# Optimization experiments

Hardware: AMD Instinct MI355X
Metric: run time of the kernel (lower is better)

The kernel has to match this reference:

```python
import jax, jax.numpy as jnp
import numpy as np

TEMPERATURE = 1.0
CLAMP = 10.0

def setup_inputs() -> dict:
    key = jax.random.key(0)
    k1, k2, kw, kb, km = jax.random.split(key, 5)
    B, N1, N2, D = 8, 2048, 2048, 256
    features1 = jax.random.normal(k1, (B, N1, D), dtype=jnp.float32)
    features2 = jax.random.normal(k2, (B, N2, D), dtype=jnp.float32)
    # Linear(D, D) params (torch convention: y = x @ W.T + b)
    W = jax.random.normal(kw, (D, D), dtype=jnp.float32) * (1.0 / np.sqrt(D))
    b = jax.random.normal(kb, (D,), dtype=jnp.float32) * 0.02
    # learnable metric matrix (initialized near identity, small perturbation)
    metric = jnp.eye(D, dtype=jnp.float32) + 0.01 * jax.random.normal(km, (D, D), dtype=jnp.float32)
    return {"features1": features1, "features2": features2, "W": W, "b": b, "metric": metric}

def reference(features1, features2, W, b, metric):
    # Linear transform (torch nn.Linear: x @ W.T + b)
    f1 = features1 @ W.T + b  # (B, N1, D)
    f2 = features2 @ W.T + b  # (B, N2, D)
    M = (metric + metric.T) * 0.5  # symmetrized metric (D, D)
    # Mahalanobis distance^2 expanded: d(x,y) = xMx + yMy - 2 xMy (valid since M symmetric)
    f1M = f1 @ M                                      # (B, N1, D)
    f2M = f2 @ M                                      # (B, N2, D)
    q1 = jnp.sum(f1M * f1, axis=-1)                   # (B, N1)
    q2 = jnp.sum(f2M * f2, axis=-1)                   # (B, N2)
    cross = jnp.einsum('bnd,bmd->bnm', f1M, f2)       # (B, N1, N2)
    dist_sq = q1[:, :, None] + q2[:, None, :] - 2.0 * cross
    stable = jnp.clip(-dist_sq / TEMPERATURE, -CLAMP, CLAMP)
    return jnp.exp(stable)
```

## Files before the change

kernel.cpp:

```cpp
#include <hip/hip_runtime.h>

#define DD 256
#define NROW 2048
#define TROWS 16384

typedef __attribute__((ext_vector_type(8))) short short8;
typedef __attribute__((ext_vector_type(4))) float f32x4;

__device__ __forceinline__ unsigned short f2bf(float f) {
  unsigned int u = __float_as_uint(f);
  u += 0x7FFFu + ((u >> 16) & 1u);
  return (unsigned short)(u >> 16);
}

__device__ __forceinline__ void gload_lds16(const unsigned short* g, unsigned short* l) {
  __builtin_amdgcn_global_load_lds(
      (const __attribute__((address_space(1))) unsigned int*)(const void*)g,
      (__attribute__((address_space(3))) unsigned int*)(void*)l,
      16, 0, 0);
}

__global__ void k_prep(const float* __restrict__ metric, const float* __restrict__ W,
                       const float* __restrict__ bvec,
                       unsigned short* __restrict__ Wbf, unsigned short* __restrict__ WpT,
                       float* __restrict__ bp)
{
  __shared__ float msrow[DD];
  __shared__ float red[DD];
  const int e = blockIdx.x, d = threadIdx.x;
  msrow[d] = 0.5f * (metric[e*DD + d] + metric[d*DD + e]);
  Wbf[e*DD + d] = f2bf(W[e*DD + d]);
  __syncthreads();
  float acc = 0.f;
  for (int j = 0; j < DD; ++j) acc += msrow[j] * W[j*DD + d];
  WpT[e*DD + d] = f2bf(acc);
  red[d] = msrow[d] * bvec[d];
  __syncthreads();
  for (int s = 128; s; s >>= 1) { if (d < s) red[d] += red[d + s]; __syncthreads(); }
  if (d == 0) bp[e] = red[0];
}

__global__ __launch_bounds__(256, 2)
void k_fgemm(const float* __restrict__ x1, const float* __restrict__ x2,
             const unsigned short* __restrict__ B1, const unsigned short* __restrict__ B2,
             const float* __restrict__ bb, const float* __restrict__ bpv,
             unsigned short* __restrict__ o1, unsigned short* __restrict__ o2,
             float* __restrict__ qp1, float* __restrict__ qp2)
{
  __shared__ __align__(16) unsigned short As[2][64*32];
  __shared__ __align__(16) unsigned short B1s[2][256*32];
  __shared__ __align__(16) unsigned short B2s[2][256*32];

  const int tid  = threadIdx.x;
  const int lane = tid & 63;
  const int wave = tid >> 6;
  const int row0 = blockIdx.x * 64;
  const int z    = blockIdx.y;

  const float* X       = z ? x2 : x1;
  unsigned short* outp = z ? o2 : o1;
  float* qp            = z ? qp2 : qp1;

  f32x4 accF[4][4], accM[4][4];
#pragma unroll
  for (int m = 0; m < 4; ++m)
#pragma unroll
    for (int n = 0; n < 4; ++n) { accF[m][n] = (f32x4){0,0,0,0}; accM[m][n] = (f32x4){0,0,0,0}; }

  const int ar = tid >> 2;
  const int ako = (tid & 3) * 8;
  const int lrow = lane >> 2;
  const int lkk  = (lane & 3) * 8;

#define STAGE_B(buf, k0) do { \
  _Pragma("unroll") \
  for (int c = 0; c < 4; ++c) { \
    const int chunk = wave * 4 + c; \
    const int rb = (chunk*16 + lrow)*DD + (k0) + lkk; \
    gload_lds16(B1 + rb, &B1s[buf][chunk*512]); \
    gload_lds16(B2 + rb, &B2s[buf][chunk*512]); \
  } } while (0)

#define LOAD_A(k0) \
  float4 a0 = *(const float4*)(X + (long long)(row0 + ar)*DD + (k0) + ako); \
  float4 a1 = *(const float4*)(X + (long long)(row0 + ar)*DD + (k0) + ako + 4)

#define CVT_WRITE_A(buf) do { \
  union { unsigned short us[8]; int4 v; } u; \
  u.us[0]=f2bf(a0.x); u.us[1]=f2bf(a0.y); u.us[2]=f2bf(a0.z); u.us[3]=f2bf(a0.w); \
  u.us[4]=f2bf(a1.x); u.us[5]=f2bf(a1.y); u.us[6]=f2bf(a1.z); u.us[7]=f2bf(a1.w); \
  *(int4*)&As[buf][ar*32 + ako] = u.v; } while (0)

  {
    LOAD_A(0);
    STAGE_B(0, 0);
    CVT_WRITE_A(0);
  }
  __syncthreads();

  const int lr = lane & 15;
  const int lk = (lane >> 4) * 8;

#pragma unroll
  for (int kt = 0; kt < 8; ++kt) {
    const int cur = kt & 1;
    if (kt < 7) {
      const int k0 = (kt + 1) * 32;
      LOAD_A(k0);
      STAGE_B(cur ^ 1, k0);
      short8 af[4];
#pragma unroll
      for (int m = 0; m < 4; ++m) af[m] = *(const short8*)&As[cur][(m*16 + lr)*32 + lk];
#pragma unroll
      for (int n = 0; n < 4; ++n) {
        const short8 b1 = *(const short8*)&B1s[cur][(wave*64 + n*16 + lr)*32 + lk];
        const short8 b2 = *(const short8*)&B2s[cur][(wave*64 + n*16 + lr)*32 + lk];
#pragma unroll
        for (int m = 0; m < 4; ++m) {
          accF[m][n] = __builtin_amdgcn_mfma_f32_16x16x32_bf16(af[m], b1, accF[m][n], 0, 0, 0);
          accM[m][n] = __builtin_amdgcn_mfma_f32_16x16x32_bf16(af[m], b2, accM[m][n], 0, 0, 0);
        }
      }
      CVT_WRITE_A(cur ^ 1);
    } else {
      short8 af[4];
#pragma unroll
      for (int m = 0; m < 4; ++m) af[m] = *(const short8*)&As[cur][(m*16 + lr)*32 + lk];
#pragma unroll
      for (int n = 0; n < 4; ++n) {
        const short8 b1 = *(const short8*)&B1s[cur][(wave*64 + n*16 + lr)*32 + lk];
        const short8 b2 = *(const short8*)&B2s[cur][(wave*64 + n*16 + lr)*32 + lk];
#pragma unroll
        for (int m = 0; m < 4; ++m) {
          accF[m][n] = __builtin_amdgcn_mfma_f32_16x16x32_bf16(af[m], b1, accF[m][n], 0, 0, 0);
          accM[m][n] = __builtin_amdgcn_mfma_f32_16x16x32_bf16(af[m], b2, accM[m][n], 0, 0, 0);
        }
      }
    }
    __syncthreads();
  }

  float bbv[4], bpv4[4];
#pragma unroll
  for (int n = 0; n < 4; ++n) {
    const int coll = wave*64 + n*16 + (lane & 15);
    bbv[n]  = bb[coll];
    bpv4[n] = bpv[coll];
  }
#pragma unroll
  for (int m = 0; m < 4; ++m) {
#pragma unroll
    for (int r = 0; r < 4; ++r) {
      const int rowl = m*16 + (lane >> 4)*4 + r;
      float p = 0.f;
#pragma unroll
      for (int n = 0; n < 4; ++n) {
        const int coll = wave*64 + n*16 + (lane & 15);
        const float fv  = accF[m][n][r] + bbv[n];
        const float fMv = accM[m][n][r] + bpv4[n];
        p += fv * fMv;
        outp[(long long)(row0 + rowl)*DD + coll] = f2bf(z ? fv : fMv);
      }
      p += __shfl_xor(p, 1); p += __shfl_xor(p, 2);
      p += __shfl_xor(p, 4); p += __shfl_xor(p, 8);
      if ((lane & 15) == 0) qp[wave*TROWS + row0 + rowl] = p;
    }
  }
#undef STAGE_B
#undef LOAD_A
#undef CVT_WRITE_A
}

__global__ __launch_bounds__(256, 2)
void k_cross(const unsigned short* __restrict__ f1M, const unsigned short* __restrict__ f2,
             const float* __restrict__ qp1, const float* __restrict__ qp2,
             float* __restrict__ out)
{
  __shared__ __align__(16) unsigned short As[2][128*32];
  __shared__ __align__(16) unsigned short Bs[2][128*32];
  __shared__ float q1s[128];
  __shared__ float q2s[128];

  const int tid  = threadIdx.x;
  const int lane = tid & 63;
  const int wave = tid >> 6;
  const int wr = wave >> 1;
  const int wc = wave & 1;

  const int bid = blockIdx.x;
  const int z  = bid & 7;
  const int t  = bid >> 3;
  const int bx = t & 15;
  const int by = t >> 4;
  const int row0 = by * 128;
  const int col0 = bx * 128;

  const unsigned short* A = f1M + (long long)z * NROW * DD;
  const unsigned short* B = f2  + (long long)z * NROW * DD;

  if (tid < 128) {
    const int rg = z*NROW + row0 + tid;
    q1s[tid] = qp1[rg] + qp1[TROWS + rg] + qp1[2*TROWS + rg] + qp1[3*TROWS + rg];
  } else {
    const int cg = z*NROW + col0 + (tid - 128);
    q2s[tid-128] = qp2[cg] + qp2[TROWS + cg] + qp2[2*TROWS + cg] + qp2[3*TROWS + cg];
  }

  f32x4 acc[4][4];
#pragma unroll
  for (int m = 0; m < 4; ++m)
#pragma unroll
    for (int n = 0; n < 4; ++n) acc[m][n] = (f32x4){0,0,0,0};

  const int lrow = lane >> 2;
  const int lkk  = (lane & 3) * 8;

#define STAGE_C(buf, k0) do { \
  _Pragma("unroll") \
  for (int c = 0; c < 2; ++c) { \
    const int chunk = wave * 2 + c; \
    gload_lds16(A + (long long)(row0 + chunk*16 + lrow)*DD + (k0) + lkk, &As[buf][chunk*512]); \
    gload_lds16(B + (long long)(col0 + chunk*16 + lrow)*DD + (k0) + lkk, &Bs[buf][chunk*512]); \
  } } while (0)

  STAGE_C(0, 0);
  __syncthreads();

  const int lr = lane & 15;
  const int lk = (lane >> 4) * 8;

#pragma unroll
  for (int kt = 0; kt < 8; ++kt) {
    const int cur = kt & 1;
    if (kt < 7) STAGE_C(cur ^ 1, (kt + 1) * 32);
    short8 af[4];
#pragma unroll
    for (int m = 0; m < 4; ++m) af[m] = *(const short8*)&As[cur][(wr*64 + m*16 + lr)*32 + lk];
#pragma unroll
    for (int n = 0; n < 4; ++n) {
      const short8 bfr = *(const short8*)&Bs[cur][(wc*64 + n*16 + lr)*32 + lk];
#pragma unroll
      for (int m = 0; m < 4; ++m)
        acc[m][n] = __builtin_amdgcn_mfma_f32_16x16x32_bf16(af[m], bfr, acc[m][n], 0, 0, 0);
    }
    __syncthreads();
  }

  float* outz = out + (long long)z * NROW * NROW;
#pragma unroll
  for (int m = 0; m < 4; ++m) {
#pragma unroll
    for (int r = 0; r < 4; ++r) {
      const int rowl = wr*64 + m*16 + (lane >> 4)*4 + r;
#pragma unroll
      for (int n = 0; n < 4; ++n) {
        const int coll = wc*64 + n*16 + (lane & 15);
        const float dsq = q1s[rowl] + q2s[coll] - 2.0f * acc[m][n][r];
        const float sc = fminf(fmaxf(-dsq, -10.0f), 10.0f);
        outz[(long long)(row0 + rowl)*NROW + (col0 + coll)] = __expf(sc);
      }
    }
  }
#undef STAGE_C
}

extern "C" void kernel_launch(void* const* d_in, const int* in_sizes, int n_in,
                              void* d_out, int out_size, void* d_ws, size_t ws_size,
                              hipStream_t stream) {
  const float* x1     = (const float*)d_in[0];
  const float* x2     = (const float*)d_in[1];
  const float* W      = (const float*)d_in[2];
  const float* bv     = (const float*)d_in[3];
  const float* metric = (const float*)d_in[4];
  float* out = (float*)d_out;

  if (ws_size < 20000000) return;
  unsigned short* p   = (unsigned short*)d_ws;
  unsigned short* f1M = p; p += (size_t)TROWS*DD;
  unsigned short* f2  = p; p += (size_t)TROWS*DD;
  unsigned short* Wbf = p; p += DD*DD;
  unsigned short* WpT = p; p += DD*DD;
  float* fp  = (float*)p;
  float* qp1 = fp; fp += 4*TROWS;
  float* qp2 = fp; fp += 4*TROWS;
  float* bp  = fp; fp += 256;

  k_prep<<<256, 256, 0, stream>>>(metric, W, bv, Wbf, WpT, bp);
  dim3 gf(256, 2);
  k_fgemm<<<gf, 256, 0, stream>>>(x1, x2, Wbf, WpT, bv, bp, f1M, f2, qp1, qp2);
  k_cross<<<2048, 256, 0, stream>>>(f1M, f2, qp1, qp2, out);
}
```

Before: 71.07 us.

## Merge three kernels into one persistent cooperative kernel with grid syncs

```diff
diff --git a/kernel.cpp b/kernel.cpp
--- a/kernel.cpp
+++ b/kernel.cpp
@@ -1,4 +1,7 @@
 #include <hip/hip_runtime.h>
+#include <hip/hip_cooperative_groups.h>
+
+namespace cg = cooperative_groups;
 
 #define DD 256
 #define NROW 2048
@@ -20,65 +23,56 @@
       16, 0, 0);
 }
 
-__global__ void k_prep(const float* __restrict__ metric, const float* __restrict__ W,
-                       const float* __restrict__ bvec,
-                       unsigned short* __restrict__ Wbf, unsigned short* __restrict__ WpT,
-                       float* __restrict__ bp)
+union SMem {
+  struct { float msrow[DD]; float red[DD]; } pr;
+  struct { unsigned short As[2][64*32]; unsigned short B1s[2][256*32]; unsigned short B2s[2][256*32]; } fg;
+  struct { unsigned short As[2][128*32]; unsigned short Bs[2][128*32]; float q1s[128]; float q2s[128]; } cr;
+};
+
+__global__ __launch_bounds__(256, 2)
+void k_mega(const float* x1, const float* x2, const float* W,
+            const float* bvec, const float* metric,
+            unsigned short* Wbf, unsigned short* WpT, float* bp,
+            unsigned short* f1M, unsigned short* f2,
+            float* qp1, float* qp2, float* out)
 {
-  __shared__ float msrow[DD];
-  __shared__ float red[DD];
-  const int e = blockIdx.x, d = threadIdx.x;
-  msrow[d] = 0.5f * (metric[e*DD + d] + metric[d*DD + e]);
-  Wbf[e*DD + d] = f2bf(W[e*DD + d]);
-  __syncthreads();
-  float acc = 0.f;
-  for (int j = 0; j < DD; ++j) acc += msrow[j] * W[j*DD + d];
-  WpT[e*DD + d] = f2bf(acc);
-  red[d] = msrow[d] * bvec[d];
-  __syncthreads();
-  for (int s = 128; s; s >>= 1) { if (d < s) red[d] += red[d + s]; __syncthreads(); }
-  if (d == 0) bp[e] = red[0];
-}
-
-__global__ __launch_bounds__(256, 2)
-void k_fgemm(const float* __restrict__ x1, const float* __restrict__ x2,
-             const unsigned short* __restrict__ B1, const unsigned short* __restrict__ B2,
-             const float* __restrict__ bb, const float* __restrict__ bpv,
-             unsigned short* __restrict__ o1, unsigned short* __restrict__ o2,
-             float* __restrict__ qp1, float* __restrict__ qp2)
-{
-  __shared__ __align__(16) unsigned short As[2][64*32];
-  __shared__ __align__(16) unsigned short B1s[2][256*32];
-  __shared__ __align__(16) unsigned short B2s[2][256*32];
-
+  __shared__ SMem sm;
   const int tid  = threadIdx.x;
   const int lane = tid & 63;
   const int wave = tid >> 6;
-  const int row0 = blockIdx.x * 64;
-  const int z    = blockIdx.y;
-
-  const float* X       = z ? x2 : x1;
-  unsigned short* outp = z ? o2 : o1;
-  float* qp            = z ? qp2 : qp1;
-
-  f32x4 accF[4][4], accM[4][4];
-#pragma unroll
-  for (int m = 0; m < 4; ++m)
-#pragma unroll
-    for (int n = 0; n < 4; ++n) { accF[m][n] = (f32x4){0,0,0,0}; accM[m][n] = (f32x4){0,0,0,0}; }
-
-  const int ar = tid >> 2;
-  const int ako = (tid & 3) * 8;
-  const int lrow = lane >> 2;
-  const int lkk  = (lane & 3) * 8;
+  const int nb   = gridDim.x;
+
+  for (int e = blockIdx.x; e < DD; e += nb) {
+    const int d = tid;
+    sm.pr.msrow[d] = 0.5f * (metric[e*DD + d] + metric[d*DD + e]);
+    Wbf[e*DD + d] = f2bf(W[e*DD + d]);
+    __syncthreads();
+    float acc = 0.f;
+    for (int j = 0; j < DD; ++j) acc += sm.pr.msrow[j] * W[j*DD + d];
+    WpT[e*DD + d] = f2bf(acc);
+    sm.pr.red[d] = sm.pr.msrow[d] * bvec[d];
+    __syncthreads();
+    for (int s = 128; s; s >>= 1) { if (d < s) sm.pr.red[d] += sm.pr.red[d + s]; __syncthreads(); }
+    if (d == 0) bp[e] = sm.pr.red[0];
+    __syncthreads();
+  }
+  cg::this_grid().sync();
+
+  {
+    const int ar   = tid >> 2;
+    const int ako  = (tid & 3) * 8;
+    const int lrow = lane >> 2;
+    const int lkk  = (lane & 3) * 8;
+    const int lr = lane & 15;
+    const int lk = (lane >> 4) * 8;
 
 #define STAGE_B(buf, k0) do { \
   _Pragma("unroll") \
   for (int c = 0; c < 4; ++c) { \
     const int chunk = wave * 4 + c; \
     const int rb = (chunk*16 + lrow)*DD + (k0) + lkk; \
-    gload_lds16(B1 + rb, &B1s[buf][chunk*512]); \
-    gload_lds16(B2 + rb, &B2s[buf][chunk*512]); \
+    gload_lds16(Wbf + rb, &sm.fg.B1s[buf][chunk*512]); \
+    gload_lds16(WpT + rb, &sm.fg.B2s[buf][chunk*512]); \
   } } while (0)
 
 #define LOAD_A(k0) \
@@ -86,182 +80,178 @@
   float4 a1 = *(const float4*)(X + (long long)(row0 + ar)*DD + (k0) + ako + 4)
 
 #define CVT_WRITE_A(buf) do { \
-  union { unsigned short us[8]; int4 v; } u; \
-  u.us[0]=f2bf(a0.x); u.us[1]=f2bf(a0.y); u.us[2]=f2bf(a0.z); u.us[3]=f2bf(a0.w); \
-  u.us[4]=f2bf(a1.x); u.us[5]=f2bf(a1.y); u.us[6]=f2bf(a1.z); u.us[7]=f2bf(a1.w); \
-  *(int4*)&As[buf][ar*32 + ako] = u.v; } while (0)
-
-  {
-    LOAD_A(0);
-    STAGE_B(0, 0);
-    CVT_WRITE_A(0);
-  }
-  __syncthreads();
-
-  const int lr = lane & 15;
-  const int lk = (lane >> 4) * 8;
-
-#pragma unroll
-  for (int kt = 0; kt < 8; ++kt) {
-    const int cur = kt & 1;
-    if (kt < 7) {
-      const int k0 = (kt + 1) * 32;
-      LOAD_A(k0);
-      STAGE_B(cur ^ 1, k0);
-      short8 af[4];
-#pragma unroll
-      for (int m = 0; m < 4; ++m) af[m] = *(const short8*)&As[cur][(m*16 + lr)*32 + lk];
-#pragma unroll
-      for (int n = 0; n < 4; ++n) {
-        const short8 b1 = *(const short8*)&B1s[cur][(wave*64 + n*16 + lr)*32 + lk];
-        const short8 b2 = *(const short8*)&B2s[cur][(wave*64 + n*16 + lr)*32 + lk];
-#pragma unroll
-        for (int m = 0; m < 4; ++m) {
-          accF[m][n] = __builtin_amdgcn_mfma_f32_16x16x32_bf16(af[m], b1, accF[m][n], 0, 0, 0);
-          accM[m][n] = __builtin_amdgcn_mfma_f32_16x16x32_bf16(af[m], b2, accM[m][n], 0, 0, 0);
-        }
-      }
-      CVT_WRITE_A(cur ^ 1);
-    } else {
-      short8 af[4];
-#pragma unroll
-      for (int m = 0; m < 4; ++m) af[m] = *(const short8*)&As[cur][(m*16 + lr)*32 + lk];
-#pragma unroll
-      for (int n = 0; n < 4; ++n) {
-        const short8 b1 = *(const short8*)&B1s[cur][(wave*64 + n*16 + lr)*32 + lk];
-        const short8 b2 = *(const short8*)&B2s[cur][(wave*64 + n*16 + lr)*32 + lk];
-#pragma unroll
-        for (int m = 0; m < 4; ++m) {
-          accF[m][n] = __builtin_amdgcn_mfma_f32_16x16x32_bf16(af[m], b1, accF[m][n], 0, 0, 0);
-          accM[m][n] = __builtin_amdgcn_mfma_f32_16x16x32_bf16(af[m], b2, accM[m][n], 0, 0, 0);
-        }
-      }
-    }
-    __syncthreads();
-  }
-
-  float bbv[4], bpv4[4];
-#pragma unroll
-  for (int n = 0; n < 4; ++n) {
-    const int coll = wave*64 + n*16 + (lane & 15);
-    bbv[n]  = bb[coll];
-    bpv4[n] = bpv[coll];
-  }
-#pragma unroll
-  for (int m = 0; m < 4; ++m) {
-#pragma unroll
-    for (int r = 0; r < 4; ++r) {
-      const int rowl = m*16 + (lane >> 4)*4 + r;
-      float p = 0.f;
+  union { unsigned short us[8]; int4 v; } uu; \
+  uu.us[0]=f2bf(a0.x); uu.us[1]=f2bf(a0.y); uu.us[2]=f2bf(a0.z); uu.us[3]=f2bf(a0.w); \
+  uu.us[4]=f2bf(a1.x); uu.us[5]=f2bf(a1.y); uu.us[6]=f2bf(a1.z); uu.us[7]=f2bf(a1.w); \
+  *(int4*)&sm.fg.As[buf][ar*32 + ako] = uu.v; } while (0)
+
+    for (int u = blockIdx.x; u < 512; u += nb) {
+      const int row0 = (u >> 1) * 64;
+      const int z    = u & 1;
+      const float* X       = z ? x2 : x1;
+      unsigned short* outp = z ? f2 : f1M;
+      float* qp            = z ? qp2 : qp1;
+
+      f32x4 accF[4][4], accM[4][4];
+#pragma unroll
+      for (int m = 0; m < 4; ++m)
+#pragma unroll
+        for (int n = 0; n < 4; ++n) { accF[m][n] = (f32x4){0,0,0,0}; accM[m][n] = (f32x4){0,0,0,0}; }
+
+      __syncthreads();
+      { LOAD_A(0); STAGE_B(0, 0); CVT_WRITE_A(0); }
+      __syncthreads();
+
+#pragma unroll
+      for (int kt = 0; kt < 8; ++kt) {
+        const int cur = kt & 1;
+        if (kt < 7) {
+          const int k0 = (kt + 1) * 32;
+          LOAD_A(k0);
+          STAGE_B(cur ^ 1, k0);
+          short8 af[4];
+#pragma unroll
+          for (int m = 0; m < 4; ++m) af[m] = *(const short8*)&sm.fg.As[cur][(m*16 + lr)*32 + lk];
+#pragma unroll
+          for (int n = 0; n < 4; ++n) {
+            const short8 b1 = *(const short8*)&sm.fg.B1s[cur][(wave*64 + n*16 + lr)*32 + lk];
+            const short8 b2 = *(const short8*)&sm.fg.B2s[cur][(wave*64 + n*16 + lr)*32 + lk];
+#pragma unroll
+            for (int m = 0; m < 4; ++m) {
+              accF[m][n] = __builtin_amdgcn_mfma_f32_16x16x32_bf16(af[m], b1, accF[m][n], 0, 0, 0);
+              accM[m][n] = __builtin_amdgcn_mfma_f32_16x16x32_bf16(af[m], b2, accM[m][n], 0, 0, 0);
+            }
+          }
+          CVT_WRITE_A(cur ^ 1);
+        } else {
+          short8 af[4];
+#pragma unroll
+          for (int m = 0; m < 4; ++m) af[m] = *(const short8*)&sm.fg.As[cur][(m*16 + lr)*32 + lk];
+#pragma unroll
+          for (int n = 0; n < 4; ++n) {
+            const short8 b1 = *(const short8*)&sm.fg.B1s[cur][(wave*64 + n*16 + lr)*32 + lk];
+            const short8 b2 = *(const short8*)&sm.fg.B2s[cur][(wave*64 + n*16 + lr)*32 + lk];
+#pragma unroll
+            for (int m = 0; m < 4; ++m) {
+              accF[m][n] = __builtin_amdgcn_mfma_f32_16x16x32_bf16(af[m], b1, accF[m][n], 0, 0, 0);
+              accM[m][n] = __builtin_amdgcn_mfma_f32_16x16x32_bf16(af[m], b2, accM[m][n], 0, 0, 0);
+            }
+          }
+        }
+        __syncthreads();
+      }
+
+      float bbv[4], bpv4[4];
 #pragma unroll
       for (int n = 0; n < 4; ++n) {
         const int coll = wave*64 + n*16 + (lane & 15);
-        const float fv  = accF[m][n][r] + bbv[n];
-        const float fMv = accM[m][n][r] + bpv4[n];
-        p += fv * fMv;
-        outp[(long long)(row0 + rowl)*DD + coll] = f2bf(z ? fv : fMv);
-      }
-      p += __shfl_xor(p, 1); p += __shfl_xor(p, 2);
-      p += __shfl_xor(p, 4); p += __shfl_xor(p, 8);
-      if ((lane & 15) == 0) qp[wave*TROWS + row0 + rowl] = p;
+        bbv[n]  = bvec[coll];
+        bpv4[n] = bp[coll];
+      }
+#pragma unroll
+      for (int m = 0; m < 4; ++m) {
+#pragma unroll
+        for (int r = 0; r < 4; ++r) {
+          const int rowl = m*16 + (lane >> 4)*4 + r;
+          float p = 0.f;
+#pragma unroll
+          for (int n = 0; n < 4; ++n) {
+            const int coll = wave*64 + n*16 + (lane & 15);
+            const float fv  = accF[m][n][r] + bbv[n];
+            const float fMv = accM[m][n][r] + bpv4[n];
+            p += fv * fMv;
+            outp[(long long)(row0 + rowl)*DD + coll] = f2bf(z ? fv : fMv);
+          }
+          p += __shfl_xor(p, 1); p += __shfl_xor(p, 2);
+          p += __shfl_xor(p, 4); p += __shfl_xor(p, 8);
+          if ((lane & 15) == 0) qp[wave*TROWS + row0 + rowl] = p;
+        }
+      }
     }
-  }
 #undef STAGE_B
 #undef LOAD_A
 #undef CVT_WRITE_A
-}
-
-__global__ __launch_bounds__(256, 2)
-void k_cross(const unsigned short* __restrict__ f1M, const unsigned short* __restrict__ f2,
-             const float* __restrict__ qp1, const float* __restrict__ qp2,
-             float* __restrict__ out)
-{
-  __shared__ __align__(16) unsigned short As[2][128*32];
-  __shared__ __align__(16) unsigned short Bs[2][128*32];
-  __shared__ float q1s[128];
-  __shared__ float q2s[128];
-
-  const int tid  = threadIdx.x;
-  const int lane = tid & 63;
-  const int wave = tid >> 6;
-  const int wr = wave >> 1;
-  const int wc = wave & 1;
-
-  const int bid = blockIdx.x;
-  const int z  = bid & 7;
-  const int t  = bid >> 3;
-  const int bx = t & 15;
-  const int by = t >> 4;
-  const int row0 = by * 128;
-  const int col0 = bx * 128;
-
-  const unsigned short* A = f1M + (long long)z * NROW * DD;
-  const unsigned short* B = f2  + (long long)z * NROW * DD;
-
-  if (tid < 128) {
-    const int rg = z*NROW + row0 + tid;
-    q1s[tid] = qp1[rg] + qp1[TROWS + rg] + qp1[2*TROWS + rg] + qp1[3*TROWS + rg];
-  } else {
-    const int cg = z*NROW + col0 + (tid - 128);
-    q2s[tid-128] = qp2[cg] + qp2[TROWS + cg] + qp2[2*TROWS + cg] + qp2[3*TROWS + cg];
   }
-
-  f32x4 acc[4][4];
-#pragma unroll
-  for (int m = 0; m < 4; ++m)
-#pragma unroll
-    for (int n = 0; n < 4; ++n) acc[m][n] = (f32x4){0,0,0,0};
-
-  const int lrow = lane >> 2;
-  const int lkk  = (lane & 3) * 8;
+  cg::this_grid().sync();
+
+  {
+    const int wr = wave >> 1;
+    const int wc = wave & 1;
+    const int lrow = lane >> 2;
+    const int lkk  = (lane & 3) * 8;
+    const int lr = lane & 15;
+    const int lk = (lane >> 4) * 8;
 
 #define STAGE_C(buf, k0) do { \
   _Pragma("unroll") \
   for (int c = 0; c < 2; ++c) { \
     const int chunk = wave * 2 + c; \
-    gload_lds16(A + (long long)(row0 + chunk*16 + lrow)*DD + (k0) + lkk, &As[buf][chunk*512]); \
-    gload_lds16(B + (long long)(col0 + chunk*16 + lrow)*DD + (k0) + lkk, &Bs[buf][chunk*512]); \
+    gload_lds16(A + (long long)(row0 + chunk*16 + lrow)*DD + (k0) + lkk, &sm.cr.As[buf][chunk*512]); \
+    gload_lds16(B + (long long)(col0 + chunk*16 + lrow)*DD + (k0) + lkk, &sm.cr.Bs[buf][chunk*512]); \
   } } while (0)
 
-  STAGE_C(0, 0);
-  __syncthreads();
-
-  const int lr = lane & 15;
-  const int lk = (lane >> 4) * 8;
-
-#pragma unroll
-  for (int kt = 0; kt < 8; ++kt) {
-    const int cur = kt & 1;
-    if (kt < 7) STAGE_C(cur ^ 1, (kt + 1) * 32);
-    short8 af[4];
-#pragma unroll
-    for (int m = 0; m < 4; ++m) af[m] = *(const short8*)&As[cur][(wr*64 + m*16 + lr)*32 + lk];
-#pragma unroll
-    for (int n = 0; n < 4; ++n) {
-      const short8 bfr = *(const short8*)&Bs[cur][(wc*64 + n*16 + lr)*32 + lk];
+    for (int w = blockIdx.x; w < 2048; w += nb) {
+      const int z  = w & 7;
+      const int t  = w >> 3;
+      const int col0 = (t & 15) * 128;
+      const int row0 = (t >> 4) * 128;
+
+      const unsigned short* A = f1M + (long long)z * NROW * DD;
+      const unsigned short* B = f2  + (long long)z * NROW * DD;
+
+      __syncthreads();
+      if (tid < 128) {
+        const int rg = z*NROW + row0 + tid;
+        sm.cr.q1s[tid] = qp1[rg] + qp1[TROWS + rg] + qp1[2*TROWS + rg] + qp1[3*TROWS + rg];
+      } else {
+        const int cg2 = z*NROW + col0 + (tid - 128);
+        sm.cr.q2s[tid-128] = qp2[cg2] + qp2[TROWS + cg2] + qp2[2*TROWS + cg2] + qp2[3*TROWS + cg2];
+      }
+
+      f32x4 acc[4][4];
 #pragma unroll
       for (int m = 0; m < 4; ++m)
-        acc[m][n] = __builtin_amdgcn_mfma_f32_16x16x32_bf16(af[m], bfr, acc[m][n], 0, 0, 0);
+#pragma unroll
+        for (int n = 0; n < 4; ++n) acc[m][n] = (f32x4){0,0,0,0};
+
+      STAGE_C(0, 0);
+      __syncthreads();
+
+#pragma unroll
+      for (int kt = 0; kt < 8; ++kt) {
+        const int cur = kt & 1;
+        if (kt < 7) STAGE_C(cur ^ 1, (kt + 1) * 32);
+        short8 af[4];
+#pragma unroll
+        for (int m = 0; m < 4; ++m) af[m] = *(const short8*)&sm.cr.As[cur][(wr*64 + m*16 + lr)*32 + lk];
+#pragma unroll
+        for (int n = 0; n < 4; ++n) {
+          const short8 bfr = *(const short8*)&sm.cr.Bs[cur][(wc*64 + n*16 + lr)*32 + lk];
+#pragma unroll
+          for (int m = 0; m < 4; ++m)
+            acc[m][n] = __builtin_amdgcn_mfma_f32_16x16x32_bf16(af[m], bfr, acc[m][n], 0, 0, 0);
+        }
+        __syncthreads();
+      }
+
+      float* outz = out + (long long)z * NROW * NROW;
+#pragma unroll
+      for (int m = 0; m < 4; ++m) {
+#pragma unroll
+        for (int r = 0; r < 4; ++r) {
+          const int rowl = wr*64 + m*16 + (lane >> 4)*4 + r;
+#pragma unroll
+          for (int n = 0; n < 4; ++n) {
+            const int coll = wc*64 + n*16 + (lane & 15);
+            const float dsq = sm.cr.q1s[rowl] + sm.cr.q2s[coll] - 2.0f * acc[m][n][r];
+            const float sc = fminf(fmaxf(-dsq, -10.0f), 10.0f);
+            outz[(long long)(row0 + rowl)*NROW + (col0 + coll)] = __expf(sc);
+          }
+        }
+      }
     }
-    __syncthreads();
+#undef STAGE_C
   }
-
-  float* outz = out + (long long)z * NROW * NROW;
-#pragma unroll
-  for (int m = 0; m < 4; ++m) {
-#pragma unroll
-    for (int r = 0; r < 4; ++r) {
-      const int rowl = wr*64 + m*16 + (lane >> 4)*4 + r;
-#pragma unroll
-      for (int n = 0; n < 4; ++n) {
-        const int coll = wc*64 + n*16 + (lane & 15);
-        const float dsq = q1s[rowl] + q2s[coll] - 2.0f * acc[m][n][r];
-        const float sc = fminf(fmaxf(-dsq, -10.0f), 10.0f);
-        outz[(long long)(row0 + rowl)*NROW + (col0 + coll)] = __expf(sc);
-      }
-    }
-  }
-#undef STAGE_C
 }
 
 extern "C" void kernel_launch(void* const* d_in, const int* in_sizes, int n_in,
@@ -285,8 +275,15 @@
   float* qp2 = fp; fp += 4*TROWS;
   float* bp  = fp; fp += 256;
 
-  k_prep<<<256, 256, 0, stream>>>(metric, W, bv, Wbf, WpT, bp);
-  dim3 gf(256, 2);
-  k_fgemm<<<gf, 256, 0, stream>>>(x1, x2, Wbf, WpT, bv, bp, f1M, f2, qp1, qp2);
-  k_cross<<<2048, 256, 0, stream>>>(f1M, f2, qp1, qp2, out);
-}
+  int maxb = 0;
+  hipOccupancyMaxActiveBlocksPerMultiprocessor(&maxb, k_mega, 256, 0);
+  int grid = maxb * 256;
+  if (grid > 512) grid = 512;
+  if (grid < 8)   grid = 8;
+
+  void* args[] = { (void*)&x1, (void*)&x2, (void*)&W, (void*)&bv, (void*)&metric,
+                   (void*)&Wbf, (void*)&WpT, (void*)&bp,
+                   (void*)&f1M, (void*)&f2,
+                   (void*)&qp1, (void*)&qp2, (void*)&out };
+  hipLaunchCooperativeKernel(k_mega, dim3(grid), dim3(256), args, 0, stream);
+}
```

New measurement: 260.3 us. 3.66x slower.
